# Kernel optimization log

Measured on AMD Instinct MI355X. Metric: run time of the kernel, lower is better.

Reference implementation:

```python
import jax, jax.numpy as jnp
import numpy as np

N_NODES = 50000
N_EDGES = 800000
N_FEAT = 128
N_CLASSES = 64
K_HOPS = 2


def setup_inputs() -> dict:
    key = jax.random.key(0)
    k1, k2, k3, k4 = jax.random.split(key, 4)
    x = jax.random.normal(k1, (N_NODES, N_FEAT), dtype=jnp.float32)
    edge_index = jax.random.randint(k2, (2, N_EDGES), 0, N_NODES, dtype=jnp.int64)
    # Linear(num_features -> num_classes) params (PyG SGConv lin layer)
    lim = 1.0 / np.sqrt(N_FEAT)
    W = jax.random.uniform(k3, (N_CLASSES, N_FEAT), minval=-lim, maxval=lim, dtype=jnp.float32)
    b = jax.random.uniform(k4, (N_CLASSES,), minval=-lim, maxval=lim, dtype=jnp.float32)
    return {"x": x, "edge_index": edge_index, "W": W, "b": b}


def reference(x, edge_index, W, b):
    N = x.shape[0]
    # gcn_norm: add self-loops, symmetric normalization deg^-1/2 A_hat deg^-1/2
    loop = jnp.arange(N, dtype=edge_index.dtype)
    src = jnp.concatenate([edge_index[0], loop])  # message sources j
    dst = jnp.concatenate([edge_index[1], loop])  # message targets i
    deg = jax.ops.segment_sum(jnp.ones_like(src, dtype=x.dtype), dst, num_segments=N)
    dinv = jnp.where(deg > 0, jax.lax.rsqrt(deg), 0.0)
    norm = dinv[src] * dinv[dst]  # [E+N]
    # K=2 hops of SpMM: out[i] = sum_{j->i} norm * x[j]
    for _ in range(K_HOPS):
        x = jax.ops.segment_sum(norm[:, None] * x[src], dst, num_segments=N)
    logits = x @ W.T + b  # [N, num_classes]
    return jax.nn.log_softmax(logits, axis=1)
```

## Files before the change

### kernel.cpp

```cpp
#include <hip/hip_runtime.h>
#include <hip/hip_fp16.h>
#include <math.h>

#define NFEAT 128
#define NCLS  64
#define RQ8   8
#define WSTR  132
#define NBLK  256
#define BSLACK 2048


typedef _Float16 h2v __attribute__((ext_vector_type(2)));

__device__ __forceinline__ float dot2acc(unsigned int hv, unsigned int wv, float c) {
#if __has_builtin(__builtin_amdgcn_fdot2)
    union { unsigned int u; h2v v; } a, bq; a.u = hv; bq.u = wv;
    return __builtin_amdgcn_fdot2(a.v, bq.v, c, false);
#else
    union { unsigned int u; __half2 h; } a, bq; a.u = hv; bq.u = wv;
    float2 fa = __half22float2(a.h), fb = __half22float2(bq.h);
    return fmaf(fa.x, fb.x, fmaf(fa.y, fb.y, c));
#endif
}

__device__ __forceinline__ void acc4(__half2 a[4], uint4 v) {
    union { uint4 u; __half2 h[4]; } c; c.u = v;
    a[0] = __hadd2(a[0], c.h[0]); a[1] = __hadd2(a[1], c.h[1]);
    a[2] = __hadd2(a[2], c.h[2]); a[3] = __hadd2(a[3], c.h[3]);
}

__device__ __forceinline__ __half2 red8(__half2 a) {
    union { __half2 h; int i; } u, v;
    u.h = a; v.i = __shfl_xor(u.i, 8);  a = __hadd2(a, v.h);
    u.h = a; v.i = __shfl_xor(u.i, 16); a = __hadd2(a, v.h);
    u.h = a; v.i = __shfl_xor(u.i, 32); a = __hadd2(a, v.h);
    return a;
}

__device__ __forceinline__ int block_excl_scan_256(int v, int tid, int* scratch, int* total) {
    const int lane = tid & 63, wv = tid >> 6;
    __syncthreads();
    int x = v;
    #pragma unroll
    for (int off = 1; off < 64; off <<= 1) {
        int y = __shfl_up(x, off);
        if (lane >= off) x += y;
    }
    if (lane == 63) scratch[wv] = x;
    __syncthreads();
    if (wv == 0 && lane < 4) {
        int t = scratch[lane];
        int y = __shfl_up(t, 1); if (lane >= 1) t += y;
        y = __shfl_up(t, 2);     if (lane >= 2) t += y;
        scratch[4 + lane] = t;
    }
    __syncthreads();
    int wbase = (wv == 0) ? 0 : scratch[4 + wv - 1];
    if (total) *total = scratch[7];
    return wbase + x - v;
}

__global__ __launch_bounds__(256) void hist_kernel(const int* __restrict__ dst,
                                                   int* __restrict__ h,
                                                   int E4, int E, int nb) {
    __shared__ int lh[256];
    const int tid = threadIdx.x;
    lh[tid] = 0;
    __syncthreads();
    for (int idx = blockIdx.x * 256 + tid; idx < E4; idx += NBLK * 256) {
        int base = idx * 4;
        if (base + 3 < E) {
            int4 d = ((const int4*)dst)[idx];
            atomicAdd(&lh[d.x >> 8], 1); atomicAdd(&lh[d.y >> 8], 1);
            atomicAdd(&lh[d.z >> 8], 1); atomicAdd(&lh[d.w >> 8], 1);
        } else {
            for (int e = base; e < E; ++e) atomicAdd(&lh[dst[e] >> 8], 1);
        }
    }
    __syncthreads();
    if (tid < nb) h[blockIdx.x * nb + tid] = lh[tid];
}

__global__ __launch_bounds__(256) void colscan_kernel(int* __restrict__ h,
                                                      int* __restrict__ btot, int nb) {
    __shared__ int scratch[8];
    const int tid = threadIdx.x;
    const int B = blockIdx.x;
    int v = h[tid * nb + B];
    int tot;
    int pre = block_excl_scan_256(v, tid, scratch, &tot);
    h[tid * nb + B] = pre;
    if (tid == 0) btot[B] = tot;
}

__global__ __launch_bounds__(256) void bucket_scatter_kernel(const int* __restrict__ src,
                                                             const int* __restrict__ dst,
                                                             const int* __restrict__ h,
                                                             const int* __restrict__ btot,
                                                             unsigned int* __restrict__ bedg,
                                                             int E4, int E, int nb) {
    __shared__ int cur[256];
    __shared__ int scratch[8];
    const int tid = threadIdx.x;
    int bt = (tid < nb) ? btot[tid] : 0;
    int pre = block_excl_scan_256(bt, tid, scratch, nullptr);
    if (tid < nb) cur[tid] = pre + h[blockIdx.x * nb + tid];
    __syncthreads();
    for (int idx = blockIdx.x * 256 + tid; idx < E4; idx += NBLK * 256) {
        int base = idx * 4;
        if (base + 3 < E) {
            int4 s = ((const int4*)src)[idx];
            int4 d = ((const int4*)dst)[idx];
            int p;
            p = atomicAdd(&cur[d.x >> 8], 1); bedg[p] = ((unsigned)s.x << 8) | (d.x & 255);
            p = atomicAdd(&cur[d.y >> 8], 1); bedg[p] = ((unsigned)s.y << 8) | (d.y & 255);
            p = atomicAdd(&cur[d.z >> 8], 1); bedg[p] = ((unsigned)s.z << 8) | (d.z & 255);
            p = atomicAdd(&cur[d.w >> 8], 1); bedg[p] = ((unsigned)s.w << 8) | (d.w & 255);
        } else {
            for (int e = base; e < E; ++e) {
                int p = atomicAdd(&cur[dst[e] >> 8], 1);
                bedg[p] = ((unsigned)src[e] << 8) | (dst[e] & 255);
            }
        }
    }
}

__global__ __launch_bounds__(256) void drain_kernel(const unsigned int* __restrict__ bedg,
                                                    const int* __restrict__ btot,
                                                    int* __restrict__ csr,
                                                    int* __restrict__ rbeg,
                                                    int* __restrict__ rend,
                                                    float* __restrict__ dinv,
                                                    int N, int nb) {
    __shared__ int lcnt[256];
    __shared__ int loc[256];
    __shared__ int scratch[8];
    __shared__ int s0_s, s1_s;
    const int B = blockIdx.x;
    const int tid = threadIdx.x;

    int bt = (tid < nb) ? btot[tid] : 0;
    int pre = block_excl_scan_256(bt, tid, scratch, nullptr);
    if (tid == B) { s0_s = pre; s1_s = pre + bt; }
    lcnt[tid] = 0;
    __syncthreads();
    const int s0 = s0_s, s1 = s1_s;

    for (int e = s0 + tid; e < s1; e += 256)
        atomicAdd(&lcnt[bedg[e] & 255u], 1);
    __syncthreads();

    const int c = lcnt[tid];
    const int cp = (c + 8) & ~7;
    int rpre = block_excl_scan_256(cp, tid, scratch, nullptr);
    const int base = s0 + BSLACK * B;
    loc[tid] = base + rpre;
    __syncthreads();
    lcnt[tid] = loc[tid];
    __syncthreads();

    for (int e = s0 + tid; e < s1; e += 256) {
        unsigned int Ev = bedg[e];
        int p = atomicAdd(&lcnt[Ev & 255u], 1);
        csr[p] = (int)(Ev >> 8);
    }
    __syncthreads();

    int i = B * 256 + tid;
    if (i < N) {
        int start = loc[tid], end = start + cp;
        int q = lcnt[tid];
        csr[q++] = i;
        for (int p = q; p < end; ++p) csr[p] = N;
        rbeg[i] = start; rend[i] = end;
        dinv[i] = rsqrtf((float)c + 1.0f);
    }
}

__global__ __launch_bounds__(512) void gemm_kernel(const float* __restrict__ x,
                                                   const float* __restrict__ W,
                                                   const float* __restrict__ dinv,
                                                   __half* __restrict__ zh,
                                                   __half* __restrict__ y1h, int N) {
    __shared__ __half Wl[NCLS * WSTR];
    __shared__ __align__(16) __half HT[64][NFEAT];

    const int tid = threadIdx.x;
    const int w = tid >> 6, lane = tid & 63;

    if (blockIdx.x == 0 && tid < 32) {
        if (tid < 16) ((uint2*)zh)[(size_t)N * 16 + tid] = uint2{0u, 0u};
        else          ((uint2*)y1h)[(size_t)N * 16 + (tid - 16)] = uint2{0u, 0u};
    }

    for (int e = tid; e < NCLS * NFEAT; e += 512) {
        int r = e >> 7, c = e & 127;
        Wl[r * WSTR + c] = __float2half(W[e]);
    }
    {
        const float4* srcf = (const float4*)(x + (size_t)blockIdx.x * 64 * NFEAT);
        uint2* dh = (uint2*)&HT[0][0];
        const int row0 = blockIdx.x * 64;
        #pragma unroll
        for (int t = 0; t < 4; ++t) {
            int e = tid + 512 * t;
            float4 f = (row0 + (e >> 5) < N) ? srcf[e] : float4{0.f, 0.f, 0.f, 0.f};
            union { uint2 u; __half2 h[2]; } r;
            r.h[0] = __floats2half2_rn(f.x, f.y);
            r.h[1] = __floats2half2_rn(f.z, f.w);
            dh[e] = r.u;
        }
    }
    __syncthreads();

    unsigned int wreg[64];
    {
        const uint2* wr = (const uint2*)&Wl[lane * WSTR];
        #pragma unroll
        for (int t = 0; t < 32; ++t) {
            uint2 v = wr[t];
            wreg[2 * t] = v.x; wreg[2 * t + 1] = v.y;
        }
    }

    #pragma unroll 1
    for (int r = 0; r < 8; ++r) {
        int node = blockIdx.x * 64 + w * 8 + r;
        if (node >= N) break;
        const unsigned int* hrow = (const unsigned int*)&HT[w * 8 + r][0];
        float dot = 0.f;
        #pragma unroll
        for (int t = 0; t < 64; ++t)
            dot = dot2acc(hrow[t], wreg[t], dot);
        zh[(size_t)node * NCLS + lane] = __float2half(dinv[node] * dot);
    }
}

__device__ __forceinline__ void gather_dual(__half2 a0[4], __half2 a1[4],
                                            const uint4* __restrict__ X,
                                            const int* __restrict__ csr,
                                            int k0, int ke0, int k1, int ke1,
                                            int sub, int q, int Nd) {
    int j00 = (k0     < ke0) ? csr[k0 + sub]     : Nd;
    int j01 = (k0 + 8 < ke0) ? csr[k0 + 8 + sub] : Nd;
    int j10 = (k1     < ke1) ? csr[k1 + sub]     : Nd;
    int j11 = (k1 + 8 < ke1) ? csr[k1 + 8 + sub] : Nd;
    while (k0 < ke0 || k1 < ke1) {
        uint4 v00 = X[(size_t)j00 * RQ8 + q];
        uint4 v01 = X[(size_t)j01 * RQ8 + q];
        uint4 v10 = X[(size_t)j10 * RQ8 + q];
        uint4 v11 = X[(size_t)j11 * RQ8 + q];
        k0 += 16; k1 += 16;
        j00 = (k0     < ke0) ? csr[k0 + sub]     : Nd;
        j01 = (k0 + 8 < ke0) ? csr[k0 + 8 + sub] : Nd;
        j10 = (k1     < ke1) ? csr[k1 + sub]     : Nd;
        j11 = (k1 + 8 < ke1) ? csr[k1 + 8 + sub] : Nd;
        acc4(a0, v00); acc4(a0, v01);
        acc4(a1, v10); acc4(a1, v11);
    }
}

__global__ __launch_bounds__(256) void hop64_dual_kernel(const __half* __restrict__ in_h,
                                                         const float* __restrict__ dinv,
                                                         const int* __restrict__ rbeg,
                                                         const int* __restrict__ rend,
                                                         const int* __restrict__ csr,
                                                         __half* __restrict__ out_h, int N) {
    const int tid = threadIdx.x;
    const int w = tid >> 6, lane = tid & 63;
    const int i0 = (blockIdx.x * 4 + w) * 2;
    if (i0 >= N) return;
    const int i1 = i0 + 1;
    const bool has1 = (i1 < N);
    const int sub = lane >> 3;
    const int q = lane & 7;
    const uint4* X = (const uint4*)in_h;

    __half2 a0[4], a1[4];
    a0[0] = __float2half2_rn(0.f); a0[1] = a0[0]; a0[2] = a0[0]; a0[3] = a0[0];
    a1[0] = a0[0]; a1[1] = a0[0]; a1[2] = a0[0]; a1[3] = a0[0];

    int ks0 = rbeg[i0], ke0 = rend[i0];
    int ks1 = has1 ? rbeg[i1] : 0, ke1 = has1 ? rend[i1] : 0;
    gather_dual(a0, a1, X, csr, ks0, ke0, ks1, ke1, sub, q, N);

    a0[0] = red8(a0[0]); a0[1] = red8(a0[1]); a0[2] = red8(a0[2]); a0[3] = red8(a0[3]);
    a1[0] = red8(a1[0]); a1[1] = red8(a1[1]); a1[2] = red8(a1[2]); a1[3] = red8(a1[3]);

    if (sub == 0) {
        {
            float di = dinv[i0];
            float s = di * di;
            union { uint4 u; __half2 h[4]; } r;
            #pragma unroll
            for (int t = 0; t < 4; ++t) {
                float2 f = __half22float2(a0[t]);
                r.h[t] = __floats2half2_rn(s * f.x, s * f.y);
            }
            ((uint4*)out_h)[(size_t)i0 * RQ8 + q] = r.u;
        }
        if (has1) {
            float di = dinv[i1];
            float s = di * di;
            union { uint4 u; __half2 h[4]; } r;
            #pragma unroll
            for (int t = 0; t < 4; ++t) {
                float2 f = __half22float2(a1[t]);
                r.h[t] = __floats2half2_rn(s * f.x, s * f.y);
            }
            ((uint4*)out_h)[(size_t)i1 * RQ8 + q] = r.u;
        }
    }
}

__device__ __forceinline__ void cls_epilogue(__half2 a[4], float di, float4 b0, float4 b1,
                                             float* __restrict__ out, int node, int q) {
    float f[8];
    float2 p;
    p = __half22float2(a[0]); f[0] = fmaf(di, p.x, b0.x); f[1] = fmaf(di, p.y, b0.y);
    p = __half22float2(a[1]); f[2] = fmaf(di, p.x, b0.z); f[3] = fmaf(di, p.y, b0.w);
    p = __half22float2(a[2]); f[4] = fmaf(di, p.x, b1.x); f[5] = fmaf(di, p.y, b1.y);
    p = __half22float2(a[3]); f[6] = fmaf(di, p.x, b1.z); f[7] = fmaf(di, p.y, b1.w);
    float m = f[0];
    #pragma unroll
    for (int t = 1; t < 8; ++t) m = fmaxf(m, f[t]);
    m = fmaxf(m, __shfl_xor(m, 1));
    m = fmaxf(m, __shfl_xor(m, 2));
    m = fmaxf(m, __shfl_xor(m, 4));
    float se = 0.f;
    #pragma unroll
    for (int t = 0; t < 8; ++t) se += __expf(f[t] - m);
    se += __shfl_xor(se, 1);
    se += __shfl_xor(se, 2);
    se += __shfl_xor(se, 4);
    float ls = m + logf(se);
    float4 o0 = {f[0] - ls, f[1] - ls, f[2] - ls, f[3] - ls};
    float4 o1 = {f[4] - ls, f[5] - ls, f[6] - ls, f[7] - ls};
    float4* op = (float4*)(out + (size_t)node * NCLS);
    op[q * 2] = o0; op[q * 2 + 1] = o1;
}

__global__ __launch_bounds__(256) void hop2cls_dual_kernel(const __half* __restrict__ in_h,
                                                           const float* __restrict__ dinv,
                                                           const int* __restrict__ rbeg,
                                                           const int* __restrict__ rend,
                                                           const int* __restrict__ csr,
                                                           const float* __restrict__ b,
                                                           float* __restrict__ out, int N) {
    const int tid = threadIdx.x;
    const int w = tid >> 6, lane = tid & 63;
    const int i0 = (blockIdx.x * 4 + w) * 2;
    if (i0 >= N) return;
    const int i1 = i0 + 1;
    const bool has1 = (i1 < N);
    const int sub = lane >> 3;
    const int q = lane & 7;
    const uint4* X = (const uint4*)in_h;

    float4 b0 = ((const float4*)b)[q * 2];
    float4 b1 = ((const float4*)b)[q * 2 + 1];

    __half2 a0[4], a1[4];
    a0[0] = __float2half2_rn(0.f); a0[1] = a0[0]; a0[2] = a0[0]; a0[3] = a0[0];
    a1[0] = a0[0]; a1[1] = a0[0]; a1[2] = a0[0]; a1[3] = a0[0];

    int ks0 = rbeg[i0], ke0 = rend[i0];
    int ks1 = has1 ? rbeg[i1] : 0, ke1 = has1 ? rend[i1] : 0;
    gather_dual(a0, a1, X, csr, ks0, ke0, ks1, ke1, sub, q, N);

    a0[0] = red8(a0[0]); a0[1] = red8(a0[1]); a0[2] = red8(a0[2]); a0[3] = red8(a0[3]);
    a1[0] = red8(a1[0]); a1[1] = red8(a1[1]); a1[2] = red8(a1[2]); a1[3] = red8(a1[3]);

    if (sub == 0) {
        cls_epilogue(a0, dinv[i0], b0, b1, out, i0, q);
        if (has1) cls_epilogue(a1, dinv[i1], b0, b1, out, i1, q);
    }
}


static inline size_t align256(size_t v) { return (v + 255) & ~(size_t)255; }

extern "C" void kernel_launch(void* const* d_in, const int* in_sizes, int n_in,
                              void* d_out, int out_size, void* d_ws, size_t ws_size,
                              hipStream_t stream) {
    const float* x  = (const float*)d_in[0];
    const int*   ei = (const int*)d_in[1];
    const float* W  = (const float*)d_in[2];
    const float* b  = (const float*)d_in[3];
    float* out = (float*)d_out;

    const int N = in_sizes[0] / NFEAT;
    const int E = in_sizes[1] / 2;
    const int* src = ei;
    const int* dst = ei + E;
    const int NBUCK = (N + 255) >> 8;

    const int CSR_CAP = E + BSLACK * NBUCK + 64;

    char* ws = (char*)d_ws;
    size_t o = 0;
    int*          h     = (int*)(ws + o);          o += align256((size_t)NBLK * NBUCK * 4);
    int*          btot  = (int*)(ws + o);          o += align256(256 * 4);
    unsigned int* bedg  = (unsigned int*)(ws + o); o += align256((size_t)E * 4);
    int*          csr   = (int*)(ws + o);          o += align256((size_t)CSR_CAP * 4);
    int*          rbeg  = (int*)(ws + o);          o += align256((size_t)N * 4);
    int*          rend  = (int*)(ws + o);          o += align256((size_t)N * 4);
    float*        dinv  = (float*)(ws + o);        o += align256((size_t)N * 4);
    __half*       zh    = (__half*)(ws + o);       o += align256((size_t)(N + 1) * NCLS * 2);
    __half*       y1h   = (__half*)(ws + o);       o += align256((size_t)(N + 1) * NCLS * 2);

    const int E4 = (E + 3) / 4;
    const int HG = (N + 7) / 8;

    hist_kernel<<<NBLK, 256, 0, stream>>>(dst, h, E4, E, NBUCK);
    colscan_kernel<<<NBUCK, 256, 0, stream>>>(h, btot, NBUCK);
    bucket_scatter_kernel<<<NBLK, 256, 0, stream>>>(src, dst, h, btot, bedg, E4, E, NBUCK);
    drain_kernel<<<NBUCK, 256, 0, stream>>>(bedg, btot, csr, rbeg, rend, dinv, N, NBUCK);
    gemm_kernel<<<(N + 63) / 64, 512, 0, stream>>>(x, W, dinv, zh, y1h, N);
    hop64_dual_kernel<<<HG, 256, 0, stream>>>(zh, dinv, rbeg, rend, csr, y1h, N);
    hop2cls_dual_kernel<<<HG, 256, 0, stream>>>(y1h, dinv, rbeg, rend, csr, b, out, N);
}
```

Before: 154.7 us.

## Fuse CSR build stages into one cooperative kernel with grid syncs

Replaces the four CSR-build launches (histogram, column scan, bucket scatter, drain) with a single cooperative kernel of 512 blocks that separates the phases with grid.sync(). The histogram grid is doubled, and the column scan now handles two rows per thread. The aim is to remove launch gaps and inter-kernel drain between the small build stages. The four-kernel path remains as a fallback if the cooperative launch fails. Grid-wide barriers and idle blocks in the nb-limited phases (about 196 of 512 blocks active) may offset the gain.

```diff
diff --git a/kernel.cpp b/kernel.cpp
--- a/kernel.cpp
+++ b/kernel.cpp
@@ -1,12 +1,16 @@
 #include <hip/hip_runtime.h>
+#include <hip/hip_cooperative_groups.h>
 #include <hip/hip_fp16.h>
 #include <math.h>
+
+namespace cg = cooperative_groups;
 
 #define NFEAT 128
 #define NCLS  64
 #define RQ8   8
 #define WSTR  132
-#define NBLK  256
+#define BGRID 512
+#define FNBLK 256
 #define BSLACK 2048
 
 
@@ -60,138 +64,136 @@
     return wbase + x - v;
 }
 
-__global__ __launch_bounds__(256) void hist_kernel(const int* __restrict__ dst,
-                                                   int* __restrict__ h,
-                                                   int E4, int E, int nb) {
-    __shared__ int lh[256];
-    const int tid = threadIdx.x;
-    lh[tid] = 0;
-    __syncthreads();
-    for (int idx = blockIdx.x * 256 + tid; idx < E4; idx += NBLK * 256) {
-        int base = idx * 4;
-        if (base + 3 < E) {
-            int4 d = ((const int4*)dst)[idx];
-            atomicAdd(&lh[d.x >> 8], 1); atomicAdd(&lh[d.y >> 8], 1);
-            atomicAdd(&lh[d.z >> 8], 1); atomicAdd(&lh[d.w >> 8], 1);
-        } else {
-            for (int e = base; e < E; ++e) atomicAdd(&lh[dst[e] >> 8], 1);
-        }
-    }
-    __syncthreads();
-    if (tid < nb) h[blockIdx.x * nb + tid] = lh[tid];
-}
-
-__global__ __launch_bounds__(256) void colscan_kernel(int* __restrict__ h,
-                                                      int* __restrict__ btot, int nb) {
-    __shared__ int scratch[8];
-    const int tid = threadIdx.x;
-    const int B = blockIdx.x;
-    int v = h[tid * nb + B];
-    int tot;
-    int pre = block_excl_scan_256(v, tid, scratch, &tot);
-    h[tid * nb + B] = pre;
-    if (tid == 0) btot[B] = tot;
-}
-
-__global__ __launch_bounds__(256) void bucket_scatter_kernel(const int* __restrict__ src,
-                                                             const int* __restrict__ dst,
-                                                             const int* __restrict__ h,
-                                                             const int* __restrict__ btot,
-                                                             unsigned int* __restrict__ bedg,
-                                                             int E4, int E, int nb) {
-    __shared__ int cur[256];
-    __shared__ int scratch[8];
-    const int tid = threadIdx.x;
-    int bt = (tid < nb) ? btot[tid] : 0;
-    int pre = block_excl_scan_256(bt, tid, scratch, nullptr);
-    if (tid < nb) cur[tid] = pre + h[blockIdx.x * nb + tid];
-    __syncthreads();
-    for (int idx = blockIdx.x * 256 + tid; idx < E4; idx += NBLK * 256) {
-        int base = idx * 4;
-        if (base + 3 < E) {
-            int4 s = ((const int4*)src)[idx];
-            int4 d = ((const int4*)dst)[idx];
-            int p;
-            p = atomicAdd(&cur[d.x >> 8], 1); bedg[p] = ((unsigned)s.x << 8) | (d.x & 255);
-            p = atomicAdd(&cur[d.y >> 8], 1); bedg[p] = ((unsigned)s.y << 8) | (d.y & 255);
-            p = atomicAdd(&cur[d.z >> 8], 1); bedg[p] = ((unsigned)s.z << 8) | (d.z & 255);
-            p = atomicAdd(&cur[d.w >> 8], 1); bedg[p] = ((unsigned)s.w << 8) | (d.w & 255);
-        } else {
-            for (int e = base; e < E; ++e) {
-                int p = atomicAdd(&cur[dst[e] >> 8], 1);
-                bedg[p] = ((unsigned)src[e] << 8) | (dst[e] & 255);
-            }
-        }
-    }
-}
-
-__global__ __launch_bounds__(256) void drain_kernel(const unsigned int* __restrict__ bedg,
-                                                    const int* __restrict__ btot,
-                                                    int* __restrict__ csr,
-                                                    int* __restrict__ rbeg,
-                                                    int* __restrict__ rend,
-                                                    float* __restrict__ dinv,
-                                                    int N, int nb) {
+
+struct BuildP {
+    const int* src; const int* dst;
+    int* h; int* btot; unsigned int* bedg; int* csr;
+    int* rbeg; int* rend; float* dinv;
+    __half* zh; __half* y1h;
+    int N, E, E4, nb;
+};
+
+__global__ __launch_bounds__(256) void build_coop_kernel(BuildP p) {
+    cg::grid_group grid = cg::this_grid();
     __shared__ int lcnt[256];
     __shared__ int loc[256];
     __shared__ int scratch[8];
-    __shared__ int s0_s, s1_s;
-    const int B = blockIdx.x;
-    const int tid = threadIdx.x;
-
-    int bt = (tid < nb) ? btot[tid] : 0;
-    int pre = block_excl_scan_256(bt, tid, scratch, nullptr);
-    if (tid == B) { s0_s = pre; s1_s = pre + bt; }
-    lcnt[tid] = 0;
-    __syncthreads();
-    const int s0 = s0_s, s1 = s1_s;
-
-    for (int e = s0 + tid; e < s1; e += 256)
-        atomicAdd(&lcnt[bedg[e] & 255u], 1);
-    __syncthreads();
-
-    const int c = lcnt[tid];
-    const int cp = (c + 8) & ~7;
-    int rpre = block_excl_scan_256(cp, tid, scratch, nullptr);
-    const int base = s0 + BSLACK * B;
-    loc[tid] = base + rpre;
-    __syncthreads();
-    lcnt[tid] = loc[tid];
-    __syncthreads();
-
-    for (int e = s0 + tid; e < s1; e += 256) {
-        unsigned int Ev = bedg[e];
-        int p = atomicAdd(&lcnt[Ev & 255u], 1);
-        csr[p] = (int)(Ev >> 8);
-    }
-    __syncthreads();
-
-    int i = B * 256 + tid;
-    if (i < N) {
-        int start = loc[tid], end = start + cp;
-        int q = lcnt[tid];
-        csr[q++] = i;
-        for (int p = q; p < end; ++p) csr[p] = N;
-        rbeg[i] = start; rend[i] = end;
-        dinv[i] = rsqrtf((float)c + 1.0f);
+    __shared__ int s01[2];
+    const int tid = threadIdx.x;
+    const int bid = blockIdx.x;
+
+    {
+        lcnt[tid] = 0;
+        __syncthreads();
+        for (int idx = bid * 256 + tid; idx < p.E4; idx += BGRID * 256) {
+            int base = idx * 4;
+            if (base + 3 < p.E) {
+                int4 d = ((const int4*)p.dst)[idx];
+                atomicAdd(&lcnt[d.x >> 8], 1); atomicAdd(&lcnt[d.y >> 8], 1);
+                atomicAdd(&lcnt[d.z >> 8], 1); atomicAdd(&lcnt[d.w >> 8], 1);
+            } else {
+                for (int e = base; e < p.E; ++e) atomicAdd(&lcnt[p.dst[e] >> 8], 1);
+            }
+        }
+        __syncthreads();
+        if (tid < p.nb) p.h[bid * p.nb + tid] = lcnt[tid];
+    }
+    __threadfence();
+    grid.sync();
+
+    if (bid < p.nb) {
+        const int B = bid;
+        int v0 = p.h[(2 * tid + 0) * p.nb + B];
+        int v1 = p.h[(2 * tid + 1) * p.nb + B];
+        int tot;
+        int pre = block_excl_scan_256(v0 + v1, tid, scratch, &tot);
+        p.h[(2 * tid + 0) * p.nb + B] = pre;
+        p.h[(2 * tid + 1) * p.nb + B] = pre + v0;
+        if (tid == 0) p.btot[B] = tot;
+    }
+    __threadfence();
+    grid.sync();
+
+    {
+        int bt = (tid < p.nb) ? p.btot[tid] : 0;
+        int pre = block_excl_scan_256(bt, tid, scratch, nullptr);
+        if (tid < p.nb) lcnt[tid] = pre + p.h[bid * p.nb + tid];
+        __syncthreads();
+        for (int idx = bid * 256 + tid; idx < p.E4; idx += BGRID * 256) {
+            int base = idx * 4;
+            if (base + 3 < p.E) {
+                int4 s = ((const int4*)p.src)[idx];
+                int4 d = ((const int4*)p.dst)[idx];
+                int q2;
+                q2 = atomicAdd(&lcnt[d.x >> 8], 1); p.bedg[q2] = ((unsigned)s.x << 8) | (d.x & 255);
+                q2 = atomicAdd(&lcnt[d.y >> 8], 1); p.bedg[q2] = ((unsigned)s.y << 8) | (d.y & 255);
+                q2 = atomicAdd(&lcnt[d.z >> 8], 1); p.bedg[q2] = ((unsigned)s.z << 8) | (d.z & 255);
+                q2 = atomicAdd(&lcnt[d.w >> 8], 1); p.bedg[q2] = ((unsigned)s.w << 8) | (d.w & 255);
+            } else {
+                for (int e = base; e < p.E; ++e) {
+                    int q2 = atomicAdd(&lcnt[p.dst[e] >> 8], 1);
+                    p.bedg[q2] = ((unsigned)p.src[e] << 8) | (p.dst[e] & 255);
+                }
+            }
+        }
+    }
+    __threadfence();
+    grid.sync();
+
+    if (bid < p.nb) {
+        const int B = bid;
+        int bt = (tid < p.nb) ? p.btot[tid] : 0;
+        int pre = block_excl_scan_256(bt, tid, scratch, nullptr);
+        if (tid == B) { s01[0] = pre; s01[1] = pre + bt; }
+        lcnt[tid] = 0;
+        __syncthreads();
+        const int s0 = s01[0], s1 = s01[1];
+
+        for (int e = s0 + tid; e < s1; e += 256)
+            atomicAdd(&lcnt[p.bedg[e] & 255u], 1);
+        __syncthreads();
+
+        const int c = lcnt[tid];
+        const int cp = (c + 8) & ~7;
+        int rpre = block_excl_scan_256(cp, tid, scratch, nullptr);
+        const int base = s0 + BSLACK * B;
+        loc[tid] = base + rpre;
+        __syncthreads();
+        lcnt[tid] = loc[tid];
+        __syncthreads();
+
+        for (int e = s0 + tid; e < s1; e += 256) {
+            unsigned int Ev = p.bedg[e];
+            int q2 = atomicAdd(&lcnt[Ev & 255u], 1);
+            p.csr[q2] = (int)(Ev >> 8);
+        }
+        __syncthreads();
+
+        int i = B * 256 + tid;
+        if (i < p.N) {
+            int start = loc[tid], end = start + cp;
+            int q2 = lcnt[tid];
+            p.csr[q2++] = i;
+            for (int pp = q2; pp < end; ++pp) p.csr[pp] = p.N;
+            p.rbeg[i] = start; p.rend[i] = end;
+            p.dinv[i] = rsqrtf((float)c + 1.0f);
+        }
+    }
+    if (bid == p.nb && tid < 32) {
+        if (tid < 16) ((uint2*)p.zh)[(size_t)p.N * 16 + tid] = uint2{0u, 0u};
+        else          ((uint2*)p.y1h)[(size_t)p.N * 16 + (tid - 16)] = uint2{0u, 0u};
     }
 }
 
 __global__ __launch_bounds__(512) void gemm_kernel(const float* __restrict__ x,
                                                    const float* __restrict__ W,
                                                    const float* __restrict__ dinv,
-                                                   __half* __restrict__ zh,
-                                                   __half* __restrict__ y1h, int N) {
+                                                   __half* __restrict__ zh, int N) {
     __shared__ __half Wl[NCLS * WSTR];
     __shared__ __align__(16) __half HT[64][NFEAT];
 
     const int tid = threadIdx.x;
     const int w = tid >> 6, lane = tid & 63;
-
-    if (blockIdx.x == 0 && tid < 32) {
-        if (tid < 16) ((uint2*)zh)[(size_t)N * 16 + tid] = uint2{0u, 0u};
-        else          ((uint2*)y1h)[(size_t)N * 16 + (tid - 16)] = uint2{0u, 0u};
-    }
 
     for (int e = tid; e < NCLS * NFEAT; e += 512) {
         int r = e >> 7, c = e & 127;
@@ -289,8 +291,7 @@
 
     if (sub == 0) {
         {
-            float di = dinv[i0];
-            float s = di * di;
+            float di = dinv[i0], s = di * di;
             union { uint4 u; __half2 h[4]; } r;
             #pragma unroll
             for (int t = 0; t < 4; ++t) {
@@ -300,8 +301,7 @@
             ((uint4*)out_h)[(size_t)i0 * RQ8 + q] = r.u;
         }
         if (has1) {
-            float di = dinv[i1];
-            float s = di * di;
+            float di = dinv[i1], s = di * di;
             union { uint4 u; __half2 h[4]; } r;
             #pragma unroll
             for (int t = 0; t < 4; ++t) {
@@ -378,6 +378,130 @@
 }
 
 
+__global__ __launch_bounds__(256) void hist_kernel(const int* __restrict__ dst,
+                                                   int* __restrict__ h,
+                                                   int E4, int E, int nb) {
+    __shared__ int lh[256];
+    const int tid = threadIdx.x;
+    lh[tid] = 0;
+    __syncthreads();
+    for (int idx = blockIdx.x * 256 + tid; idx < E4; idx += FNBLK * 256) {
+        int base = idx * 4;
+        if (base + 3 < E) {
+            int4 d = ((const int4*)dst)[idx];
+            atomicAdd(&lh[d.x >> 8], 1); atomicAdd(&lh[d.y >> 8], 1);
+            atomicAdd(&lh[d.z >> 8], 1); atomicAdd(&lh[d.w >> 8], 1);
+        } else {
+            for (int e = base; e < E; ++e) atomicAdd(&lh[dst[e] >> 8], 1);
+        }
+    }
+    __syncthreads();
+    if (tid < nb) h[blockIdx.x * nb + tid] = lh[tid];
+}
+
+__global__ __launch_bounds__(256) void colscan_kernel(int* __restrict__ h,
+                                                      int* __restrict__ btot, int nb) {
+    __shared__ int scratch[8];
+    const int tid = threadIdx.x;
+    const int B = blockIdx.x;
+    int v = h[tid * nb + B];
+    int tot;
+    int pre = block_excl_scan_256(v, tid, scratch, &tot);
+    h[tid * nb + B] = pre;
+    if (tid == 0) btot[B] = tot;
+}
+
+__global__ __launch_bounds__(256) void bucket_scatter_kernel(const int* __restrict__ src,
+                                                             const int* __restrict__ dst,
+                                                             const int* __restrict__ h,
+                                                             const int* __restrict__ btot,
+                                                             unsigned int* __restrict__ bedg,
+                                                             int E4, int E, int nb) {
+    __shared__ int cur[256];
+    __shared__ int scratch[8];
+    const int tid = threadIdx.x;
+    int bt = (tid < nb) ? btot[tid] : 0;
+    int pre = block_excl_scan_256(bt, tid, scratch, nullptr);
+    if (tid < nb) cur[tid] = pre + h[blockIdx.x * nb + tid];
+    __syncthreads();
+    for (int idx = blockIdx.x * 256 + tid; idx < E4; idx += FNBLK * 256) {
+        int base = idx * 4;
+        if (base + 3 < E) {
+            int4 s = ((const int4*)src)[idx];
+            int4 d = ((const int4*)dst)[idx];
+            int p;
+            p = atomicAdd(&cur[d.x >> 8], 1); bedg[p] = ((unsigned)s.x << 8) | (d.x & 255);
+            p = atomicAdd(&cur[d.y >> 8], 1); bedg[p] = ((unsigned)s.y << 8) | (d.y & 255);
+            p = atomicAdd(&cur[d.z >> 8], 1); bedg[p] = ((unsigned)s.z << 8) | (d.z & 255);
+            p = atomicAdd(&cur[d.w >> 8], 1); bedg[p] = ((unsigned)s.w << 8) | (d.w & 255);
+        } else {
+            for (int e = base; e < E; ++e) {
+                int p = atomicAdd(&cur[dst[e] >> 8], 1);
+                bedg[p] = ((unsigned)src[e] << 8) | (dst[e] & 255);
+            }
+        }
+    }
+}
+
+__global__ __launch_bounds__(256) void drain_kernel(const unsigned int* __restrict__ bedg,
+                                                    const int* __restrict__ btot,
+                                                    int* __restrict__ csr,
+                                                    int* __restrict__ rbeg,
+                                                    int* __restrict__ rend,
+                                                    float* __restrict__ dinv,
+                                                    __half* __restrict__ zh,
+                                                    __half* __restrict__ y1h,
+                                                    int N, int nb) {
+    __shared__ int lcnt[256];
+    __shared__ int loc[256];
+    __shared__ int scratch[8];
+    __shared__ int s0_s, s1_s;
+    const int B = blockIdx.x;
+    const int tid = threadIdx.x;
+
+    int bt = (tid < nb) ? btot[tid] : 0;
+    int pre = block_excl_scan_256(bt, tid, scratch, nullptr);
+    if (tid == B) { s0_s = pre; s1_s = pre + bt; }
+    lcnt[tid] = 0;
+    __syncthreads();
+    const int s0 = s0_s, s1 = s1_s;
+
+    for (int e = s0 + tid; e < s1; e += 256)
+        atomicAdd(&lcnt[bedg[e] & 255u], 1);
+    __syncthreads();
+
+    const int c = lcnt[tid];
+    const int cp = (c + 8) & ~7;
+    int rpre = block_excl_scan_256(cp, tid, scratch, nullptr);
+    const int base = s0 + BSLACK * B;
+    loc[tid] = base + rpre;
+    __syncthreads();
+    lcnt[tid] = loc[tid];
+    __syncthreads();
+
+    for (int e = s0 + tid; e < s1; e += 256) {
+        unsigned int Ev = bedg[e];
+        int p = atomicAdd(&lcnt[Ev & 255u], 1);
+        csr[p] = (int)(Ev >> 8);
+    }
+    __syncthreads();
+
+    int i = B * 256 + tid;
+    if (i < N) {
+        int start = loc[tid], end = start + cp;
+        int q = lcnt[tid];
+        csr[q++] = i;
+        for (int p = q; p < end; ++p) csr[p] = N;
+        rbeg[i] = start; rend[i] = end;
+        dinv[i] = rsqrtf((float)c + 1.0f);
+    }
+    if (B == 0 && tid < 32) {
+        if (tid < 16) ((uint2*)zh)[(size_t)N * 16 + tid] = uint2{0u, 0u};
+        else          ((uint2*)y1h)[(size_t)N * 16 + (tid - 16)] = uint2{0u, 0u};
+    }
+}
+
+
 static inline size_t align256(size_t v) { return (v + 255) & ~(size_t)255; }
 
 extern "C" void kernel_launch(void* const* d_in, const int* in_sizes, int n_in,
@@ -399,7 +523,7 @@
 
     char* ws = (char*)d_ws;
     size_t o = 0;
-    int*          h     = (int*)(ws + o);          o += align256((size_t)NBLK * NBUCK * 4);
+    int*          h     = (int*)(ws + o);          o += align256((size_t)BGRID * NBUCK * 4);
     int*          btot  = (int*)(ws + o);          o += align256(256 * 4);
     unsigned int* bedg  = (unsigned int*)(ws + o); o += align256((size_t)E * 4);
     int*          csr   = (int*)(ws + o);          o += align256((size_t)CSR_CAP * 4);
@@ -412,11 +536,25 @@
     const int E4 = (E + 3) / 4;
     const int HG = (N + 7) / 8;
 
-    hist_kernel<<<NBLK, 256, 0, stream>>>(dst, h, E4, E, NBUCK);
-    colscan_kernel<<<NBUCK, 256, 0, stream>>>(h, btot, NBUCK);
-    bucket_scatter_kernel<<<NBLK, 256, 0, stream>>>(src, dst, h, btot, bedg, E4, E, NBUCK);
-    drain_kernel<<<NBUCK, 256, 0, stream>>>(bedg, btot, csr, rbeg, rend, dinv, N, NBUCK);
-    gemm_kernel<<<(N + 63) / 64, 512, 0, stream>>>(x, W, dinv, zh, y1h, N);
+    BuildP p;
+    p.src = src; p.dst = dst;
+    p.h = h; p.btot = btot; p.bedg = bedg; p.csr = csr;
+    p.rbeg = rbeg; p.rend = rend; p.dinv = dinv;
+    p.zh = zh; p.y1h = y1h;
+    p.N = N; p.E = E; p.E4 = E4; p.nb = NBUCK;
+
+    void* args[] = { &p };
+    hipError_t err = hipLaunchCooperativeKernel((const void*)build_coop_kernel,
+                                                dim3(BGRID), dim3(256), args, 0, stream);
+    if (err != hipSuccess) {
+        hist_kernel<<<FNBLK, 256, 0, stream>>>(dst, h, E4, E, NBUCK);
+        colscan_kernel<<<NBUCK, 256, 0, stream>>>(h, btot, NBUCK);
+        bucket_scatter_kernel<<<FNBLK, 256, 0, stream>>>(src, dst, h, btot, bedg, E4, E, NBUCK);
+        drain_kernel<<<NBUCK, 256, 0, stream>>>(bedg, btot, csr, rbeg, rend, dinv,
+                                                zh, y1h, N, NBUCK);
+    }
+
+    gemm_kernel<<<(N + 63) / 64, 512, 0, stream>>>(x, W, dinv, zh, N);
     hop64_dual_kernel<<<HG, 256, 0, stream>>>(zh, dinv, rbeg, rend, csr, y1h, N);
     hop2cls_dual_kernel<<<HG, 256, 0, stream>>>(y1h, dinv, rbeg, rend, csr, b, out, N);
 }
```

Result: slower. 510.1 us (+229.8%).

## Fuse CSR build into single per-bucket kernel scanning all edges

Applied to the files above, without the earlier changes.

Replaces the histogram, column scan, bucket scatter and drain kernels with one kernel where each block scans the entire edge list, keeps only edges whose destination falls in its 256-node bucket, buffers them in shared memory and builds its CSR slice at a fixed capacity offset. Zeroing of the padding rows moves from the GEMM kernel into this build kernel. This removes three launches and the global intermediate bucket arrays, but makes every block read the full dst array and assumes each bucket has at most a fixed number of edges.

```diff
diff --git a/kernel.cpp b/kernel.cpp
--- a/kernel.cpp
+++ b/kernel.cpp
@@ -6,8 +6,8 @@
 #define NCLS  64
 #define RQ8   8
 #define WSTR  132
-#define NBLK  256
-#define BSLACK 2048
+#define BCAP  8192
+#define ECAP  8192
 
 
 typedef _Float16 h2v __attribute__((ext_vector_type(2)));
@@ -60,138 +60,103 @@
     return wbase + x - v;
 }
 
-__global__ __launch_bounds__(256) void hist_kernel(const int* __restrict__ dst,
-                                                   int* __restrict__ h,
-                                                   int E4, int E, int nb) {
-    __shared__ int lh[256];
+__global__ __launch_bounds__(256) void build1_kernel(const int* __restrict__ src,
+                                                     const int* __restrict__ dst,
+                                                     int* __restrict__ csr,
+                                                     int* __restrict__ rbeg,
+                                                     int* __restrict__ rend,
+                                                     float* __restrict__ dinv,
+                                                     __half* __restrict__ zh,
+                                                     __half* __restrict__ y1h,
+                                                     int N, int E, int E4) {
+    __shared__ unsigned int ebuf[ECAP];
+    __shared__ int lcnt[256];
+    __shared__ int scratch[8];
+    __shared__ int ecnt_s;
     const int tid = threadIdx.x;
-    lh[tid] = 0;
-    __syncthreads();
-    for (int idx = blockIdx.x * 256 + tid; idx < E4; idx += NBLK * 256) {
+    const int B = blockIdx.x;
+
+    lcnt[tid] = 0;
+    if (tid == 0) ecnt_s = 0;
+    __syncthreads();
+
+    for (int idx = tid; idx < E4; idx += 256) {
         int base = idx * 4;
         if (base + 3 < E) {
             int4 d = ((const int4*)dst)[idx];
-            atomicAdd(&lh[d.x >> 8], 1); atomicAdd(&lh[d.y >> 8], 1);
-            atomicAdd(&lh[d.z >> 8], 1); atomicAdd(&lh[d.w >> 8], 1);
-        } else {
-            for (int e = base; e < E; ++e) atomicAdd(&lh[dst[e] >> 8], 1);
-        }
-    }
-    __syncthreads();
-    if (tid < nb) h[blockIdx.x * nb + tid] = lh[tid];
-}
-
-__global__ __launch_bounds__(256) void colscan_kernel(int* __restrict__ h,
-                                                      int* __restrict__ btot, int nb) {
-    __shared__ int scratch[8];
-    const int tid = threadIdx.x;
-    const int B = blockIdx.x;
-    int v = h[tid * nb + B];
-    int tot;
-    int pre = block_excl_scan_256(v, tid, scratch, &tot);
-    h[tid * nb + B] = pre;
-    if (tid == 0) btot[B] = tot;
-}
-
-__global__ __launch_bounds__(256) void bucket_scatter_kernel(const int* __restrict__ src,
-                                                             const int* __restrict__ dst,
-                                                             const int* __restrict__ h,
-                                                             const int* __restrict__ btot,
-                                                             unsigned int* __restrict__ bedg,
-                                                             int E4, int E, int nb) {
-    __shared__ int cur[256];
-    __shared__ int scratch[8];
-    const int tid = threadIdx.x;
-    int bt = (tid < nb) ? btot[tid] : 0;
-    int pre = block_excl_scan_256(bt, tid, scratch, nullptr);
-    if (tid < nb) cur[tid] = pre + h[blockIdx.x * nb + tid];
-    __syncthreads();
-    for (int idx = blockIdx.x * 256 + tid; idx < E4; idx += NBLK * 256) {
-        int base = idx * 4;
-        if (base + 3 < E) {
-            int4 s = ((const int4*)src)[idx];
-            int4 d = ((const int4*)dst)[idx];
-            int p;
-            p = atomicAdd(&cur[d.x >> 8], 1); bedg[p] = ((unsigned)s.x << 8) | (d.x & 255);
-            p = atomicAdd(&cur[d.y >> 8], 1); bedg[p] = ((unsigned)s.y << 8) | (d.y & 255);
-            p = atomicAdd(&cur[d.z >> 8], 1); bedg[p] = ((unsigned)s.z << 8) | (d.z & 255);
-            p = atomicAdd(&cur[d.w >> 8], 1); bedg[p] = ((unsigned)s.w << 8) | (d.w & 255);
+            if ((d.x >> 8) == B) {
+                int p = atomicAdd(&ecnt_s, 1);
+                if (p < ECAP) { ebuf[p] = ((unsigned)src[base + 0] << 8) | (d.x & 255);
+                                atomicAdd(&lcnt[d.x & 255], 1); }
+            }
+            if ((d.y >> 8) == B) {
+                int p = atomicAdd(&ecnt_s, 1);
+                if (p < ECAP) { ebuf[p] = ((unsigned)src[base + 1] << 8) | (d.y & 255);
+                                atomicAdd(&lcnt[d.y & 255], 1); }
+            }
+            if ((d.z >> 8) == B) {
+                int p = atomicAdd(&ecnt_s, 1);
+                if (p < ECAP) { ebuf[p] = ((unsigned)src[base + 2] << 8) | (d.z & 255);
+                                atomicAdd(&lcnt[d.z & 255], 1); }
+            }
+            if ((d.w >> 8) == B) {
+                int p = atomicAdd(&ecnt_s, 1);
+                if (p < ECAP) { ebuf[p] = ((unsigned)src[base + 3] << 8) | (d.w & 255);
+                                atomicAdd(&lcnt[d.w & 255], 1); }
+            }
         } else {
             for (int e = base; e < E; ++e) {
-                int p = atomicAdd(&cur[dst[e] >> 8], 1);
-                bedg[p] = ((unsigned)src[e] << 8) | (dst[e] & 255);
-            }
-        }
-    }
-}
-
-__global__ __launch_bounds__(256) void drain_kernel(const unsigned int* __restrict__ bedg,
-                                                    const int* __restrict__ btot,
-                                                    int* __restrict__ csr,
-                                                    int* __restrict__ rbeg,
-                                                    int* __restrict__ rend,
-                                                    float* __restrict__ dinv,
-                                                    int N, int nb) {
-    __shared__ int lcnt[256];
-    __shared__ int loc[256];
-    __shared__ int scratch[8];
-    __shared__ int s0_s, s1_s;
-    const int B = blockIdx.x;
-    const int tid = threadIdx.x;
-
-    int bt = (tid < nb) ? btot[tid] : 0;
-    int pre = block_excl_scan_256(bt, tid, scratch, nullptr);
-    if (tid == B) { s0_s = pre; s1_s = pre + bt; }
-    lcnt[tid] = 0;
-    __syncthreads();
-    const int s0 = s0_s, s1 = s1_s;
-
-    for (int e = s0 + tid; e < s1; e += 256)
-        atomicAdd(&lcnt[bedg[e] & 255u], 1);
-    __syncthreads();
-
+                int dv = dst[e];
+                if ((dv >> 8) == B) {
+                    int p = atomicAdd(&ecnt_s, 1);
+                    if (p < ECAP) { ebuf[p] = ((unsigned)src[e] << 8) | (dv & 255);
+                                    atomicAdd(&lcnt[dv & 255], 1); }
+                }
+            }
+        }
+    }
+    __syncthreads();
+    const int ecnt = (ecnt_s < ECAP) ? ecnt_s : ECAP;
+
+    const int i = B * 256 + tid;
     const int c = lcnt[tid];
-    const int cp = (c + 8) & ~7;
+    const int cp = (i < N) ? ((c + 8) & ~7) : 0;
     int rpre = block_excl_scan_256(cp, tid, scratch, nullptr);
-    const int base = s0 + BSLACK * B;
-    loc[tid] = base + rpre;
-    __syncthreads();
-    lcnt[tid] = loc[tid];
-    __syncthreads();
-
-    for (int e = s0 + tid; e < s1; e += 256) {
-        unsigned int Ev = bedg[e];
+    const int start = B * BCAP + rpre;
+    __syncthreads();
+    lcnt[tid] = start;
+    __syncthreads();
+
+    for (int e = tid; e < ecnt; e += 256) {
+        unsigned int Ev = ebuf[e];
         int p = atomicAdd(&lcnt[Ev & 255u], 1);
         csr[p] = (int)(Ev >> 8);
     }
     __syncthreads();
 
-    int i = B * 256 + tid;
     if (i < N) {
-        int start = loc[tid], end = start + cp;
+        int end = start + cp;
         int q = lcnt[tid];
         csr[q++] = i;
         for (int p = q; p < end; ++p) csr[p] = N;
         rbeg[i] = start; rend[i] = end;
         dinv[i] = rsqrtf((float)c + 1.0f);
     }
+    if (B == 0 && tid < 32) {
+        if (tid < 16) ((uint2*)zh)[(size_t)N * 16 + tid] = uint2{0u, 0u};
+        else          ((uint2*)y1h)[(size_t)N * 16 + (tid - 16)] = uint2{0u, 0u};
+    }
 }
 
 __global__ __launch_bounds__(512) void gemm_kernel(const float* __restrict__ x,
                                                    const float* __restrict__ W,
                                                    const float* __restrict__ dinv,
-                                                   __half* __restrict__ zh,
-                                                   __half* __restrict__ y1h, int N) {
+                                                   __half* __restrict__ zh, int N) {
     __shared__ __half Wl[NCLS * WSTR];
     __shared__ __align__(16) __half HT[64][NFEAT];
 
     const int tid = threadIdx.x;
     const int w = tid >> 6, lane = tid & 63;
-
-    if (blockIdx.x == 0 && tid < 32) {
-        if (tid < 16) ((uint2*)zh)[(size_t)N * 16 + tid] = uint2{0u, 0u};
-        else          ((uint2*)y1h)[(size_t)N * 16 + (tid - 16)] = uint2{0u, 0u};
-    }
 
     for (int e = tid; e < NCLS * NFEAT; e += 512) {
         int r = e >> 7, c = e & 127;
@@ -289,8 +254,7 @@
 
     if (sub == 0) {
         {
-            float di = dinv[i0];
-            float s = di * di;
+            float di = dinv[i0], s = di * di;
             union { uint4 u; __half2 h[4]; } r;
             #pragma unroll
             for (int t = 0; t < 4; ++t) {
@@ -300,8 +264,7 @@
             ((uint4*)out_h)[(size_t)i0 * RQ8 + q] = r.u;
         }
         if (has1) {
-            float di = dinv[i1];
-            float s = di * di;
+            float di = dinv[i1], s = di * di;
             union { uint4 u; __half2 h[4]; } r;
             #pragma unroll
             for (int t = 0; t < 4; ++t) {
@@ -395,28 +358,21 @@
     const int* dst = ei + E;
     const int NBUCK = (N + 255) >> 8;
 
-    const int CSR_CAP = E + BSLACK * NBUCK + 64;
-
     char* ws = (char*)d_ws;
     size_t o = 0;
-    int*          h     = (int*)(ws + o);          o += align256((size_t)NBLK * NBUCK * 4);
-    int*          btot  = (int*)(ws + o);          o += align256(256 * 4);
-    unsigned int* bedg  = (unsigned int*)(ws + o); o += align256((size_t)E * 4);
-    int*          csr   = (int*)(ws + o);          o += align256((size_t)CSR_CAP * 4);
-    int*          rbeg  = (int*)(ws + o);          o += align256((size_t)N * 4);
-    int*          rend  = (int*)(ws + o);          o += align256((size_t)N * 4);
-    float*        dinv  = (float*)(ws + o);        o += align256((size_t)N * 4);
-    __half*       zh    = (__half*)(ws + o);       o += align256((size_t)(N + 1) * NCLS * 2);
-    __half*       y1h   = (__half*)(ws + o);       o += align256((size_t)(N + 1) * NCLS * 2);
+    int*    csr   = (int*)(ws + o);    o += align256((size_t)NBUCK * BCAP * 4 + 256);
+    int*    rbeg  = (int*)(ws + o);    o += align256((size_t)N * 4);
+    int*    rend  = (int*)(ws + o);    o += align256((size_t)N * 4);
+    float*  dinv  = (float*)(ws + o);  o += align256((size_t)N * 4);
+    __half* zh    = (__half*)(ws + o); o += align256((size_t)(N + 1) * NCLS * 2);
+    __half* y1h   = (__half*)(ws + o); o += align256((size_t)(N + 1) * NCLS * 2);
 
     const int E4 = (E + 3) / 4;
     const int HG = (N + 7) / 8;
 
-    hist_kernel<<<NBLK, 256, 0, stream>>>(dst, h, E4, E, NBUCK);
-    colscan_kernel<<<NBUCK, 256, 0, stream>>>(h, btot, NBUCK);
-    bucket_scatter_kernel<<<NBLK, 256, 0, stream>>>(src, dst, h, btot, bedg, E4, E, NBUCK);
-    drain_kernel<<<NBUCK, 256, 0, stream>>>(bedg, btot, csr, rbeg, rend, dinv, N, NBUCK);
-    gemm_kernel<<<(N + 63) / 64, 512, 0, stream>>>(x, W, dinv, zh, y1h, N);
+    build1_kernel<<<NBUCK, 256, 0, stream>>>(src, dst, csr, rbeg, rend, dinv,
+                                             zh, y1h, N, E, E4);
+    gemm_kernel<<<(N + 63) / 64, 512, 0, stream>>>(x, W, dinv, zh, N);
     hop64_dual_kernel<<<HG, 256, 0, stream>>>(zh, dinv, rbeg, rend, csr, y1h, N);
     hop2cls_dual_kernel<<<HG, 256, 0, stream>>>(y1h, dinv, rbeg, rend, csr, b, out, N);
 }
```

Measured after the change: 553.3 us. 258% more time.
